# Kernel optimization log

Measured on AMD Instinct MI355X. Metric: run time of the kernel, lower is better.

## Reference

```python
import jax, jax.numpy as jnp
import numpy as np

MODES = 16
WIDTH = 20


def _spectral_conv(x, w_re, w_im):
    # x: (B, C, S) real. Truncated-mode spectral conv: rfft -> keep MODES ->
    # complex channel mixing -> irfft with zero-padded spectrum (numpy irfft
    # zero-pads the input spectrum to n//2+1, matching the torch zero-init out_ft).
    S = x.shape[-1]
    x_ft = jnp.fft.rfft(x, axis=-1)                      # (B, C, S//2+1) complex
    W = w_re + 1j * w_im                                  # (Cin, Cout, MODES)
    out_modes = jnp.einsum('bim,iom->bom', x_ft[:, :, :MODES], W)
    return jnp.fft.irfft(out_modes, n=S, axis=-1)         # (B, Cout, S) real


def _fno(x, point_data,
         fc0_w, fc0_b,
         sw0_re, sw0_im, w0_w, w0_b,
         sw1_re, sw1_im, w1_w, w1_b,
         sw2_re, sw2_im, w2_w, w2_b,
         sw3_re, sw3_im, w3_w, w3_b,
         fc1_w, fc1_b, fc2_w, fc2_b):
    B, S, _ = x.shape
    grid = (point_data / jnp.max(point_data)).reshape(1, S, 1)
    grid = jnp.broadcast_to(grid, (B, S, 1))
    h = jnp.concatenate([x, grid], axis=-1)               # (B, S, 2)
    h = h @ fc0_w + fc0_b                                 # (B, S, W)
    h = jnp.transpose(h, (0, 2, 1))                       # (B, W, S)
    for (sre, sim, ww, wb) in ((sw0_re, sw0_im, w0_w, w0_b),
                               (sw1_re, sw1_im, w1_w, w1_b),
                               (sw2_re, sw2_im, w2_w, w2_b),
                               (sw3_re, sw3_im, w3_w, w3_b)):
        h1 = _spectral_conv(h, sre, sim)
        h2 = jnp.einsum('bcx,oc->box', h, ww) + wb[None, :, None]  # 1x1 conv
        h = jax.nn.gelu(h1 + h2, approximate=False)
    # last layer has no gelu in torch code? It does: only first 3 followed by gelu.
    # Correction handled below.
    return h


def _fno_full(x, point_data,
              fc0_w, fc0_b,
              sw0_re, sw0_im, w0_w, w0_b,
              sw1_re, sw1_im, w1_w, w1_b,
              sw2_re, sw2_im, w2_w, w2_b,
              sw3_re, sw3_im, w3_w, w3_b,
              fc1_w, fc1_b, fc2_w, fc2_b):
    B, S, _ = x.shape
    grid = (point_data / jnp.max(point_data)).reshape(1, S, 1)
    grid = jnp.broadcast_to(grid, (B, S, 1))
    h = jnp.concatenate([x, grid], axis=-1)               # (B, S, 2)
    h = h @ fc0_w + fc0_b                                 # (B, S, W)
    h = jnp.transpose(h, (0, 2, 1))                       # (B, W, S)
    layers = ((sw0_re, sw0_im, w0_w, w0_b),
              (sw1_re, sw1_im, w1_w, w1_b),
              (sw2_re, sw2_im, w2_w, w2_b),
              (sw3_re, sw3_im, w3_w, w3_b))
    for i, (sre, sim, ww, wb) in enumerate(layers):
        h1 = _spectral_conv(h, sre, sim)
        h2 = jnp.einsum('bcx,oc->box', h, ww) + wb[None, :, None]
        h = h1 + h2
        if i < 3:  # torch: gelu after layers 0,1,2 but NOT after layer 3
            h = jax.nn.gelu(h, approximate=False)
    h = jnp.transpose(h, (0, 2, 1))                       # (B, S, W)
    h = jax.nn.gelu(h @ fc1_w + fc1_b, approximate=False)  # (B, S, 128)
    return h @ fc2_w + fc2_b                               # (B, S, 1)


def setup_inputs() -> dict:
    key = jax.random.key(0)
    ks = jax.random.split(key, 32)
    B, S, W, M, H = 32, 65536, WIDTH, MODES, 128
    scale = 1.0 / (W * W)
    d = {
        'x': jax.random.normal(ks[0], (B, S, 1), dtype=jnp.float32),
        'point_data': jax.random.uniform(ks[1], (S,), dtype=jnp.float32),
        'fc0_w': jax.random.normal(ks[2], (2, W), dtype=jnp.float32) * 0.5,
        'fc0_b': jnp.zeros((W,), dtype=jnp.float32),
        'fc1_w': jax.random.normal(ks[3], (W, H), dtype=jnp.float32) * (1.0 / np.sqrt(W)),
        'fc1_b': jnp.zeros((H,), dtype=jnp.float32),
        'fc2_w': jax.random.normal(ks[4], (H, 1), dtype=jnp.float32) * (1.0 / np.sqrt(H)),
        'fc2_b': jnp.zeros((1,), dtype=jnp.float32),
    }
    for i in range(4):
        d[f'sw{i}_re'] = scale * jax.random.uniform(ks[5 + 4 * i], (W, W, M), dtype=jnp.float32)
        d[f'sw{i}_im'] = scale * jax.random.uniform(ks[6 + 4 * i], (W, W, M), dtype=jnp.float32)
        d[f'w{i}_w'] = jax.random.normal(ks[7 + 4 * i], (W, W), dtype=jnp.float32) * (1.0 / np.sqrt(W))
        d[f'w{i}_b'] = jnp.zeros((W,), dtype=jnp.float32)
    return d


def reference(x, point_data,
              fc0_w, fc0_b,
              sw0_re, sw0_im, w0_w, w0_b,
              sw1_re, sw1_im, w1_w, w1_b,
              sw2_re, sw2_im, w2_w, w2_b,
              sw3_re, sw3_im, w3_w, w3_b,
              fc1_w, fc1_b, fc2_w, fc2_b):
    return _fno_full(x, point_data,
                     fc0_w, fc0_b,
                     sw0_re, sw0_im, w0_w, w0_b,
                     sw1_re, sw1_im, w1_w, w1_b,
                     sw2_re, sw2_im, w2_w, w2_b,
                     sw3_re, sw3_im, w3_w, w3_b,
                     fc1_w, fc1_b, fc2_w, fc2_b)
```

## Files before the change

kernel.cpp:

```cpp
#include <hip/hip_runtime.h>
#include <math.h>

#define BB 32
#define SS 65536
#define CC 20
#define NM 16
#define HH 128
#define SP 256
#define WP 64
#define NSLOT 16
#define HREC 12

using short8  = __attribute__((ext_vector_type(8))) short;
using floatx4 = __attribute__((ext_vector_type(4))) float;
using floatx2 = __attribute__((ext_vector_type(2))) float;

__device__ __forceinline__ unsigned short f2bf(float f) {
    union { float f; unsigned u; } v; v.f = f;
    unsigned u = v.u;
    return (unsigned short)((u + 0x7FFFu + ((u >> 16) & 1u)) >> 16);
}
__device__ __forceinline__ float bf2f(unsigned short h) {
    union { unsigned u; float f; } v; v.u = ((unsigned)h) << 16; return v.f;
}
__device__ __forceinline__ unsigned short f2bflo(float a) {
    return f2bf(a - bf2f(f2bf(a)));
}
__device__ __forceinline__ unsigned pk2(unsigned short lo, unsigned short hi) {
    return (unsigned)lo | ((unsigned)hi << 16);
}
__device__ __forceinline__ float asf(unsigned u) {
    union { unsigned u; float f; } v; v.u = u; return v.f;
}
__device__ __forceinline__ unsigned cvtpk(float lo, float hi) {
    unsigned r;
    asm("v_cvt_pk_bf16_f32 %0, %1, %2" : "=v"(r) : "v"(lo), "v"(hi));
    return r;
}

__device__ __forceinline__ float gelu_fast(float v) {
    float u = v * v;
    float inner = v * fmaf(0.0356774081f, u, 0.7978845608f);
    float e = __builtin_amdgcn_exp2f(inner * 2.8853900818f);
    float r = __builtin_amdgcn_rcpf(e + 1.0f);
    return fmaf(-v, r, v);
}

__device__ __forceinline__ floatx2 gelu2(floatx2 v) {
    floatx2 u = v * v;
    floatx2 inner = v * (u * 0.0356774081f + 0.7978845608f);
    floatx2 z = inner * 2.8853900818f;
    floatx2 e, r;
    e.x = __builtin_amdgcn_exp2f(z.x);
    e.y = __builtin_amdgcn_exp2f(z.y);
    r.x = __builtin_amdgcn_rcpf(e.x + 1.0f);
    r.y = __builtin_amdgcn_rcpf(e.y + 1.0f);
    return v - v * r;
}

__device__ __forceinline__ float row16_sum(float p) {
    union { float f; int i; } v, w;
    v.f = p;
    w.i = __builtin_amdgcn_update_dpp(0, v.i, 0x121, 0xF, 0xF, true); v.f += w.f;
    w.i = __builtin_amdgcn_update_dpp(0, v.i, 0x122, 0xF, 0xF, true); v.f += w.f;
    w.i = __builtin_amdgcn_update_dpp(0, v.i, 0x124, 0xF, 0xF, true); v.f += w.f;
    w.i = __builtin_amdgcn_update_dpp(0, v.i, 0x128, 0xF, 0xF, true); v.f += w.f;
    return v.f;
}

__device__ __forceinline__ int swzi(int row, int scol) {
    return row * SP + ((((scol >> 3) ^ row) & 7) << 3) + (scol & 7);
}

__device__ __forceinline__ void stage_A(unsigned short* AST, int tid,
                                        const unsigned* hw,
                                        uint4 tc0, uint4 tc1, uint4 ts0, uint4 ts1) {
    int sw = tid & 7;
    unsigned* base = (unsigned*)(AST + tid * 64);
    *(uint4*)(base + ((0 ^ sw) << 2)) = (uint4){hw[0], hw[1], hw[2], hw[3]};
    *(uint4*)(base + ((1 ^ sw) << 2)) = (uint4){hw[4], hw[5], hw[6], hw[7]};
    *(uint4*)(base + ((2 ^ sw) << 2)) = (uint4){hw[8], hw[9], 0x00003F80u, 0u};
    *(uint4*)(base + ((3 ^ sw) << 2)) = (uint4){0u, 0u, 0u, 0u};
    *(uint4*)(base + ((4 ^ sw) << 2)) = tc0;
    *(uint4*)(base + ((5 ^ sw) << 2)) = tc1;
    *(uint4*)(base + ((6 ^ sw) << 2)) = ts0;
    *(uint4*)(base + ((7 ^ sw) << 2)) = ts1;
}

__global__ __launch_bounds__(256) void k_prep(const float* __restrict__ pd,
                                              const float* __restrict__ w1,
                                              const float* __restrict__ b1f,
                                              float* __restrict__ invmax,
                                              float* __restrict__ cP,
                                              unsigned short* __restrict__ w1Tg,
                                              unsigned* __restrict__ trigT) {
    int bx = blockIdx.x;
    if (bx == 0) {
        __shared__ float red[256];
        int t = threadIdx.x;
        float m = -1e30f;
        for (int i = t; i < SS; i += 256) m = fmaxf(m, pd[i]);
        red[t] = m; __syncthreads();
        for (int off = 128; off > 0; off >>= 1) {
            if (t < off) red[t] = fmaxf(red[t], red[t + off]);
            __syncthreads();
        }
        if (t == 0) invmax[0] = 1.0f / red[0];
    } else if (bx <= 1280) {
        int idx = (bx - 1) * 256 + threadIdx.x;
        float4 z = {0.f, 0.f, 0.f, 0.f};
        ((float4*)cP)[idx] = z;
    } else if (bx == 1281) {
        for (int idx = threadIdx.x; idx < HH * 64; idx += 256) {
            int j = idx >> 6, k = idx & 63;
            unsigned short r = 0;
            if (k < CC) r = f2bf(w1[k * HH + j]);
            else if (k == CC) r = f2bf(b1f[j]);
            else if (k >= 32 && k < 32 + CC) r = f2bflo(w1[(k - 32) * HH + j]);
            else if (k == 32 + CC) r = f2bflo(b1f[j]);
            w1Tg[idx] = r;
        }
    } else {
        int s = (bx - 1282) * 256 + threadIdx.x;
        float u = (float)s * (1.0f / 32768.0f);
        float s1, c1; sincospif(u, &s1, &c1);
        float cm = 1.0f, sm = 0.0f;
        unsigned short ch[NM], sh[NM];
        #pragma unroll
        for (int m = 0; m < NM; ++m) {
            ch[m] = f2bf(cm); sh[m] = f2bf(sm);
            float cn = cm * c1 - sm * s1;
            sm = sm * c1 + cm * s1;
            cm = cn;
        }
        uint4* row = (uint4*)(trigT + (size_t)s * 16);
        row[0] = (uint4){pk2(ch[0],ch[1]), pk2(ch[2],ch[3]), pk2(ch[4],ch[5]), pk2(ch[6],ch[7])};
        row[1] = (uint4){pk2(ch[8],ch[9]), pk2(ch[10],ch[11]), pk2(ch[12],ch[13]), pk2(ch[14],ch[15])};
        row[2] = (uint4){pk2(sh[0],sh[1]), pk2(sh[2],sh[3]), pk2(sh[4],sh[5]), pk2(sh[6],sh[7])};
        row[3] = (uint4){pk2(sh[8],sh[9]), pk2(sh[10],sh[11]), pk2(sh[12],sh[13]), pk2(sh[14],sh[15])};
    }
}

__device__ __forceinline__ void dft_phase(unsigned short* sh_hA, unsigned short* sh_ph,
                                          int tid, float* cPdst) {
    int wave = tid >> 6, lane = tid & 63;
    int quad = lane >> 4, frow = lane & 15;
    floatx4 acc00 = {0.f,0.f,0.f,0.f}, acc01 = {0.f,0.f,0.f,0.f};
    floatx4 acc10 = {0.f,0.f,0.f,0.f}, acc11 = {0.f,0.f,0.f,0.f};
    int kb = wave * 64 + quad * 8;
    #pragma unroll
    for (int kc = 0; kc < 2; ++kc) {
        int k = kb + kc * 32;
        int co = (((k >> 3) ^ frow) & 7) << 3;
        short8 a0 = *(const short8*)(sh_hA + frow * SP + co);
        short8 a1 = *(const short8*)(sh_hA + (16 + frow) * SP + co);
        short8 bc = *(const short8*)(sh_ph + frow * SP + co);
        short8 bs = *(const short8*)(sh_ph + (16 + frow) * SP + co);
        acc00 = __builtin_amdgcn_mfma_f32_16x16x32_bf16(a0, bc, acc00, 0, 0, 0);
        acc01 = __builtin_amdgcn_mfma_f32_16x16x32_bf16(a0, bs, acc01, 0, 0, 0);
        acc10 = __builtin_amdgcn_mfma_f32_16x16x32_bf16(a1, bc, acc10, 0, 0, 0);
        acc11 = __builtin_amdgcn_mfma_f32_16x16x32_bf16(a1, bs, acc11, 0, 0, 0);
    }
    __syncthreads();
    float* red = (float*)sh_hA;
    #pragma unroll
    for (int r = 0; r < 4; ++r) {
        red[wave * 1024 + 0 * 256 + r * 64 + lane] = acc00[r];
        red[wave * 1024 + 1 * 256 + r * 64 + lane] = acc01[r];
        red[wave * 1024 + 2 * 256 + r * 64 + lane] = acc10[r];
        red[wave * 1024 + 3 * 256 + r * 64 + lane] = acc11[r];
    }
    __syncthreads();
    #pragma unroll
    for (int ii = 0; ii < 4; ++ii) {
        int idx = ii * 256 + tid;
        float v = red[idx] + red[1024 + idx] + red[2048 + idx] + red[3072 + idx];
        int f = idx >> 8;
        int r = (idx >> 6) & 3, ln = idx & 63;
        int o = (f >> 1) * 16 + (ln >> 4) * 4 + r;
        int m = ln & 15;
        if (o < CC) atomicAdd(cPdst + (f & 1) * 320 + o * 16 + m, v);
    }
}

__global__ __launch_bounds__(256, 4) void k_fc0_dft(const float* __restrict__ x,
        const float* __restrict__ pd, const float* __restrict__ w,
        const float* __restrict__ bias, const float* __restrict__ invmax,
        const unsigned* __restrict__ trigT,
        unsigned* __restrict__ h2, float* __restrict__ cP0) {
    __shared__ __align__(16) unsigned short LB[2 * 32 * SP];
    unsigned short* sh_hA = LB;
    unsigned short* sh_ph = LB + 32 * SP;
    int tid = threadIdx.x;
    int b = blockIdx.y;
    int s = blockIdx.x * 256 + tid;
    float xv = x[(size_t)b * SS + s];
    float g  = pd[s] * invmax[0];
    const uint4* trow = (const uint4*)(trigT + (size_t)s * 16);
    uint4 tc0 = trow[0], tc1 = trow[1], ts0 = trow[2], ts1 = trow[3];
    unsigned c8[8] = {tc0.x, tc0.y, tc0.z, tc0.w, tc1.x, tc1.y, tc1.z, tc1.w};
    unsigned s8[8] = {ts0.x, ts0.y, ts0.z, ts0.w, ts1.x, ts1.y, ts1.z, ts1.w};
    #pragma unroll
    for (int m = 0; m < NM; ++m) {
        unsigned cd = c8[m >> 1], sd = s8[m >> 1];
        sh_ph[swzi(m, tid)]      = (unsigned short)((m & 1) ? (cd >> 16) : (cd & 0xFFFFu));
        sh_ph[swzi(16 + m, tid)] = (unsigned short)((m & 1) ? (sd >> 16) : (sd & 0xFFFFu));
    }
    unsigned hv[CC / 2];
    #pragma unroll
    for (int p = 0; p < CC / 2; ++p) {
        int c0 = 2 * p, c1i = 2 * p + 1;
        floatx2 wv = {w[c0], w[c1i]};
        floatx2 gv = {w[CC + c0], w[CC + c1i]};
        floatx2 bv = {bias[c0], bias[c1i]};
        floatx2 v = wv * xv + gv * g + bv;
        unsigned dw = cvtpk(v.x, v.y);
        hv[p] = dw;
        sh_hA[swzi(c0, tid)]  = (unsigned short)(dw & 0xFFFFu);
        sh_hA[swzi(c1i, tid)] = (unsigned short)(dw >> 16);
    }
    unsigned* hp2 = h2 + ((size_t)b * SS + s) * HREC;
    *(uint4*)(hp2)     = (uint4){hv[0], hv[1], hv[2], hv[3]};
    *(uint4*)(hp2 + 4) = (uint4){hv[4], hv[5], hv[6], hv[7]};
    *(uint2*)(hp2 + 8) = make_uint2(hv[8], hv[9]);
    __syncthreads();
    dft_phase(sh_hA, sh_ph, tid, cP0 + ((size_t)(blockIdx.x & (NSLOT - 1)) * BB + b) * 640);
}

__global__ __launch_bounds__(256, 4) void k_point_dft(unsigned* __restrict__ h2,
        const unsigned short* __restrict__ Bpk,
        const unsigned* __restrict__ trigT,
        float* __restrict__ cPn) {
    __shared__ __align__(16) unsigned short LB[2 * 32 * SP];
    unsigned short* AST   = LB;
    unsigned short* sh_hA = LB;
    unsigned short* sh_ph = LB + 32 * SP;
    int tid = threadIdx.x;
    int b = blockIdx.y;
    int s = blockIdx.x * 256 + tid;

    const uint4* trow = (const uint4*)(trigT + (size_t)s * 16);
    uint4 tc0 = trow[0], tc1 = trow[1], ts0 = trow[2], ts1 = trow[3];
    const unsigned* hp2r = h2 + ((size_t)b * SS + s) * HREC;
    uint4 h03 = *(const uint4*)(hp2r);
    uint4 h47 = *(const uint4*)(hp2r + 4);
    uint2 h89 = *(const uint2*)(hp2r + 8);
    unsigned hw[CC / 2] = {h03.x, h03.y, h03.z, h03.w, h47.x, h47.y, h47.z, h47.w, h89.x, h89.y};
    stage_A(AST, tid, hw, tc0, tc1, ts0, ts1);

    int wave = tid >> 6, lane = tid & 63, col = lane & 15, quad = lane >> 4;
    const unsigned short* Bp = Bpk + (size_t)b * 4096;
    short8 wh0[2], wh1[2], wl0[2], wl1[2];
    #pragma unroll
    for (int cht = 0; cht < 2; ++cht) {
        int o = cht * 16 + col;
        wh0[cht] = *(const short8*)(Bp + o * 64 + quad * 8);
        wh1[cht] = *(const short8*)(Bp + o * 64 + 32 + quad * 8);
        wl0[cht] = *(const short8*)(Bp + 2048 + o * 64 + quad * 8);
        wl1[cht] = *(const short8*)(Bp + 2048 + o * 64 + 32 + quad * 8);
    }
    unsigned* h2b = h2 + ((size_t)b * SS + blockIdx.x * 256) * HREC;
    unsigned pkr[2][4][2];
    #pragma unroll
    for (int st = 0; st < 4; ++st) {
        int ar = wave * 64 + st * 16 + col;
        int sw = ar & 7;
        const unsigned short* abase = AST + ar * 64;
        short8 ah0 = *(const short8*)(abase + ((quad ^ sw) << 3));
        short8 ah1 = *(const short8*)(abase + (((4 + quad) ^ sw) << 3));
        #pragma unroll
        for (int cht = 0; cht < 2; ++cht) {
            floatx4 a = {0.f, 0.f, 0.f, 0.f};
            a = __builtin_amdgcn_mfma_f32_16x16x32_bf16(wh0[cht], ah0, a, 0, 0, 0);
            a = __builtin_amdgcn_mfma_f32_16x16x32_bf16(wh1[cht], ah1, a, 0, 0, 0);
            a = __builtin_amdgcn_mfma_f32_16x16x32_bf16(wl0[cht], ah0, a, 0, 0, 0);
            a = __builtin_amdgcn_mfma_f32_16x16x32_bf16(wl1[cht], ah1, a, 0, 0, 0);
            floatx2 g01 = gelu2((floatx2){a[0], a[1]});
            floatx2 g23 = gelu2((floatx2){a[2], a[3]});
            unsigned d0 = cvtpk(g01.x, g01.y);
            unsigned d1 = cvtpk(g23.x, g23.y);
            pkr[cht][st][0] = d0;
            pkr[cht][st][1] = d1;
            int p = cht * 8 + quad * 2;
            if (p < CC / 2) {
                *(uint2*)(h2b + (size_t)ar * HREC + p) = make_uint2(d0, d1);
            }
        }
    }
    __syncthreads();

    {
        unsigned c8[8] = {tc0.x, tc0.y, tc0.z, tc0.w, tc1.x, tc1.y, tc1.z, tc1.w};
        unsigned s8[8] = {ts0.x, ts0.y, ts0.z, ts0.w, ts1.x, ts1.y, ts1.z, ts1.w};
        #pragma unroll
        for (int m = 0; m < NM; ++m) {
            unsigned cd = c8[m >> 1], sd = s8[m >> 1];
            sh_ph[swzi(m, tid)]      = (unsigned short)((m & 1) ? (cd >> 16) : (cd & 0xFFFFu));
            sh_ph[swzi(16 + m, tid)] = (unsigned short)((m & 1) ? (sd >> 16) : (sd & 0xFFFFu));
        }
    }
    #pragma unroll
    for (int cht = 0; cht < 2; ++cht) {
        int ob = cht * 16 + quad * 4;
        if (ob < CC) {
            #pragma unroll
            for (int st = 0; st < 4; ++st) {
                int s_loc = wave * 64 + st * 16 + col;
                #pragma unroll
                for (int rp = 0; rp < 2; ++rp) {
                    unsigned d = pkr[cht][st][rp];
                    sh_hA[swzi(ob + 2 * rp, s_loc)]     = (unsigned short)(d & 0xFFFFu);
                    sh_hA[swzi(ob + 2 * rp + 1, s_loc)] = (unsigned short)(d >> 16);
                }
            }
        }
    }
    __syncthreads();
    dft_phase(sh_hA, sh_ph, tid, cPn + ((size_t)(blockIdx.x & (NSLOT - 1)) * BB + b) * 640);
}

__global__ __launch_bounds__(320) void k_mix(const float* __restrict__ cP,
                                             const float* __restrict__ wre, const float* __restrict__ wim,
                                             const float* __restrict__ ww, const float* __restrict__ wb,
                                             float* __restrict__ cA, float* __restrict__ cB,
                                             unsigned short* __restrict__ Bpk) {
    int b = blockIdx.x, tid = threadIdx.x;
    __shared__ float PQ[640];
    const float* base = cP + (size_t)b * 640;
    int i = tid >> 4, m = tid & 15;
    float sP = 0.f, sQ = 0.f;
    #pragma unroll 4
    for (int sl = 0; sl < NSLOT; ++sl) {
        sP += base[(size_t)sl * BB * 640 + tid];
        sQ += base[(size_t)sl * BB * 640 + 320 + tid];
    }
    PQ[i * 32 + m]      = sP;
    PQ[i * 32 + 16 + m] = sQ;
    __syncthreads();
    int o = i;
    float reY = 0.f, imY = 0.f;
    #pragma unroll
    for (int c = 0; c < CC; ++c) {
        float P = PQ[c * 32 + m], Q = PQ[c * 32 + 16 + m];
        float wr = wre[(size_t)(c * CC + o) * NM + m];
        float wi = wim[(size_t)(c * CC + o) * NM + m];
        reY += P * wr + Q * wi;
        imY += P * wi - Q * wr;
    }
    const float invS = 1.0f / (float)SS;
    float a, bb;
    if (m == 0) { a = reY * invS; bb = 0.0f; }
    else        { a = 2.0f * reY * invS; bb = -2.0f * imY * invS; }
    cA[(size_t)(b * CC + o) * NM + m] = a;
    cB[(size_t)(b * CC + o) * NM + m] = bb;

    unsigned short* Bp = Bpk + (size_t)b * 4096;
    for (int idx = tid; idx < 640; idx += 320) {
        int o8 = idx >> 5, k = idx & 31;
        float v = 0.f;
        if (k < CC) v = ww[o8 * CC + k];
        else if (k == CC) v = wb[o8];
        Bp[o8 * 64 + k]        = f2bf(v);
        Bp[2048 + o8 * 64 + k] = f2bflo(v);
    }
    for (int idx = tid; idx < 768; idx += 320) {
        int o8 = 20 + (idx >> 6), k = idx & 63;
        Bp[o8 * 64 + k] = 0;
        Bp[2048 + o8 * 64 + k] = 0;
    }
    Bp[o * 64 + 32 + m]        = f2bf(a);
    Bp[o * 64 + 48 + m]        = f2bf(bb);
    Bp[2048 + o * 64 + 32 + m] = f2bflo(a);
    Bp[2048 + o * 64 + 48 + m] = f2bflo(bb);
}

__global__ __launch_bounds__(128, 4) void k_point_final(const unsigned* __restrict__ h2,
        const unsigned short* __restrict__ Bpk,
        const unsigned short* __restrict__ w1Tg,
        const float* __restrict__ w2, const float* __restrict__ b2,
        const unsigned* __restrict__ trigT,
        float* __restrict__ out) {
    __shared__ __align__(16) unsigned short AST[128 * 64];
    unsigned short* hT = AST;
    int tid = threadIdx.x;
    int b = blockIdx.y;
    int s = blockIdx.x * 128 + tid;

    const uint4* trow = (const uint4*)(trigT + (size_t)s * 16);
    uint4 tc0 = trow[0], tc1 = trow[1], ts0 = trow[2], ts1 = trow[3];
    const unsigned* hp2r = h2 + ((size_t)b * SS + s) * HREC;
    uint4 h03 = *(const uint4*)(hp2r);
    uint4 h47 = *(const uint4*)(hp2r + 4);
    uint2 h89 = *(const uint2*)(hp2r + 8);
    unsigned hw[CC / 2] = {h03.x, h03.y, h03.z, h03.w, h47.x, h47.y, h47.z, h47.w, h89.x, h89.y};
    stage_A(AST, tid, hw, tc0, tc1, ts0, ts1);

    int wave = tid >> 6, lane = tid & 63, col = lane & 15, quad = lane >> 4;
    const unsigned short* Bp = Bpk + (size_t)b * 4096;
    short8 wh0[2], wh1[2], wl0[2], wl1[2];
    #pragma unroll
    for (int cht = 0; cht < 2; ++cht) {
        int o = cht * 16 + col;
        wh0[cht] = *(const short8*)(Bp + o * 64 + quad * 8);
        wh1[cht] = *(const short8*)(Bp + o * 64 + 32 + quad * 8);
        wl0[cht] = *(const short8*)(Bp + 2048 + o * 64 + quad * 8);
        wl1[cht] = *(const short8*)(Bp + 2048 + o * 64 + 32 + quad * 8);
    }
    float res[2][4][4];
    #pragma unroll
    for (int st = 0; st < 4; ++st) {
        int ar = wave * 64 + st * 16 + col;
        int sw = ar & 7;
        const unsigned short* abase = AST + ar * 64;
        short8 ah0 = *(const short8*)(abase + ((quad ^ sw) << 3));
        short8 ah1 = *(const short8*)(abase + (((4 + quad) ^ sw) << 3));
        #pragma unroll
        for (int cht = 0; cht < 2; ++cht) {
            floatx4 a = {0.f, 0.f, 0.f, 0.f};
            a = __builtin_amdgcn_mfma_f32_16x16x32_bf16(wh0[cht], ah0, a, 0, 0, 0);
            a = __builtin_amdgcn_mfma_f32_16x16x32_bf16(wh1[cht], ah1, a, 0, 0, 0);
            a = __builtin_amdgcn_mfma_f32_16x16x32_bf16(wl0[cht], ah0, a, 0, 0, 0);
            a = __builtin_amdgcn_mfma_f32_16x16x32_bf16(wl1[cht], ah1, a, 0, 0, 0);
            #pragma unroll
            for (int r = 0; r < 4; ++r) res[cht][st][r] = a[r];
        }
    }

    #pragma unroll
    for (int cht = 0; cht < 2; ++cht) {
        #pragma unroll
        for (int st = 0; st < 4; ++st) {
            int row = wave * 64 + st * 16 + col;
            int sw = row & 7;
            unsigned* rb = (unsigned*)(hT + row * WP);
            #pragma unroll
            for (int rp = 0; rp < 2; ++rp) {
                int dwi = cht * 8 + quad * 2 + rp;
                if (dwi <= CC / 2) {
                    float f0, f1;
                    if (dwi == CC / 2) { f0 = 1.0f; f1 = 0.0f; }
                    else { f0 = res[cht][st][2 * rp]; f1 = res[cht][st][2 * rp + 1]; }
                    unsigned hd = cvtpk(f0, f1);
                    float r0 = asf(hd << 16), r1 = asf(hd & 0xFFFF0000u);
                    unsigned ld = cvtpk(f0 - r0, f1 - r1);
                    int chunk = dwi >> 2, pos = dwi & 3;
                    rb[((chunk ^ sw) << 2) + pos]       = hd;
                    rb[(((chunk + 4) ^ sw) << 2) + pos] = ld;
                }
            }
        }
    }

    short8 bhi[8], blo[8];
    #pragma unroll
    for (int nt = 0; nt < 8; ++nt) {
        bhi[nt] = *(const short8*)(w1Tg + (size_t)(nt * 16 + col) * 64 + quad * 8);
        blo[nt] = *(const short8*)(w1Tg + (size_t)(nt * 16 + col) * 64 + 32 + quad * 8);
    }
    float w2r[8];
    #pragma unroll
    for (int nt = 0; nt < 8; ++nt) w2r[nt] = w2[nt * 16 + col];
    float b2v = b2[0];
    #pragma unroll
    for (int mt = 0; mt < 4; ++mt) {
        int srow = wave * 64 + mt * 16 + col;
        int sw = srow & 7;
        short8 ahi = *(const short8*)(hT + srow * WP + ((quad ^ sw) << 3));
        short8 alo = *(const short8*)(hT + srow * WP + (((quad ^ sw) ^ 4) << 3));
        float part[4] = {0.f, 0.f, 0.f, 0.f};
        #pragma unroll
        for (int nt = 0; nt < 8; ++nt) {
            floatx4 a = {0.f, 0.f, 0.f, 0.f};
            a = __builtin_amdgcn_mfma_f32_16x16x32_bf16(ahi, bhi[nt], a, 0, 0, 0);
            a = __builtin_amdgcn_mfma_f32_16x16x32_bf16(ahi, blo[nt], a, 0, 0, 0);
            a = __builtin_amdgcn_mfma_f32_16x16x32_bf16(alo, bhi[nt], a, 0, 0, 0);
            #pragma unroll
            for (int r = 0; r < 4; ++r) {
                float t = gelu_fast(a[r]);
                part[r] += t * w2r[nt];
            }
        }
        #pragma unroll
        for (int r = 0; r < 4; ++r) {
            float p = row16_sum(part[r]);
            if (col == 0) {
                int row = wave * 64 + mt * 16 + quad * 4 + r;
                *(float*)(&hT[row * WP + ((row & 7) << 3)]) = p + b2v;
            }
        }
    }
    __syncthreads();
    out[(size_t)b * SS + blockIdx.x * 128 + tid] = *(const float*)(&hT[tid * WP + ((tid & 7) << 3)]);
}

extern "C" void kernel_launch(void* const* d_in, const int* in_sizes, int n_in,
                              void* d_out, int out_size, void* d_ws, size_t ws_size,
                              hipStream_t stream) {
    (void)in_sizes; (void)n_in; (void)out_size; (void)ws_size;
    const float* x    = (const float*)d_in[0];
    const float* pd   = (const float*)d_in[1];
    const float* fc0w = (const float*)d_in[2];
    const float* fc0b = (const float*)d_in[3];
    const float* fc1w = (const float*)d_in[4];
    const float* fc1b = (const float*)d_in[5];
    const float* fc2w = (const float*)d_in[6];
    const float* fc2b = (const float*)d_in[7];

    char* ws = (char*)d_ws;
    unsigned* h2 = (unsigned*)ws;
    size_t off = (size_t)BB * SS * HREC * 4;
    float* cP = (float*)(ws + off); off += (size_t)4 * NSLOT * BB * 640 * 4;
    float* cA = (float*)(ws + off); off += (size_t)BB * CC * NM * 4;
    float* cB = (float*)(ws + off); off += (size_t)BB * CC * NM * 4;
    float* invmax = (float*)(ws + off); off += 256;
    unsigned short* w1Tg = (unsigned short*)(ws + off); off += (size_t)HH * 64 * 2;
    unsigned short* Bpk  = (unsigned short*)(ws + off); off += (size_t)BB * 4096 * 2;
    unsigned* trigT = (unsigned*)(ws + off); off += (size_t)SS * 16 * 4;
    const size_t CPL = (size_t)NSLOT * BB * 640;

    dim3 gBS(SS / 256, BB);
    dim3 gBF(SS / 128, BB);

    k_prep<<<1538, 256, 0, stream>>>(pd, fc1w, fc1b, invmax, cP, w1Tg, trigT);
    k_fc0_dft<<<gBS, 256, 0, stream>>>(x, pd, fc0w, fc0b, invmax, trigT, h2, cP);

    for (int l = 0; l < 3; ++l) {
        const float* wre = (const float*)d_in[8 + 4 * l];
        const float* wim = (const float*)d_in[9 + 4 * l];
        const float* ww  = (const float*)d_in[10 + 4 * l];
        const float* wb  = (const float*)d_in[11 + 4 * l];
        k_mix<<<BB, 320, 0, stream>>>(cP + (size_t)l * CPL, wre, wim, ww, wb, cA, cB, Bpk);
        k_point_dft<<<gBS, 256, 0, stream>>>(h2, Bpk, trigT, cP + (size_t)(l + 1) * CPL);
    }
    {
        const float* wre = (const float*)d_in[20];
        const float* wim = (const float*)d_in[21];
        const float* ww  = (const float*)d_in[22];
        const float* wb  = (const float*)d_in[23];
        k_mix<<<BB, 320, 0, stream>>>(cP + (size_t)3 * CPL, wre, wim, ww, wb, cA, cB, Bpk);
        k_point_final<<<gBF, 128, 0, stream>>>(h2, Bpk, w1Tg, fc2w, fc2b, trigT, (float*)d_out);
    }
}
```

Measured before the change: 505.8 us.

## Process four 256-point chunks per block, accumulating DFT partials in registers

The fc0 and point-DFT kernels now loop over four consecutive 256-point chunks inside each block. MFMA accumulators carry across chunks, so the shared-memory reduction and global atomicAdds run once per block instead of once per chunk. The grid shrinks by four, which cuts launch tail and atomic contention on the partial slots. In exchange there are fewer blocks for latency hiding and serialized syncthreads between chunks within a block.

```diff
diff --git a/kernel.cpp b/kernel.cpp
--- a/kernel.cpp
+++ b/kernel.cpp
@@ -10,6 +10,7 @@
 #define WP 64
 #define NSLOT 16
 #define HREC 12
+#define CH 4
 
 using short8  = __attribute__((ext_vector_type(8))) short;
 using floatx4 = __attribute__((ext_vector_type(4))) float;
@@ -141,12 +142,12 @@
     }
 }
 
-__device__ __forceinline__ void dft_phase(unsigned short* sh_hA, unsigned short* sh_ph,
-                                          int tid, float* cPdst) {
+__device__ __forceinline__ void dft_mfma(const unsigned short* sh_hA,
+                                         const unsigned short* sh_ph, int tid,
+                                         floatx4& acc00, floatx4& acc01,
+                                         floatx4& acc10, floatx4& acc11) {
     int wave = tid >> 6, lane = tid & 63;
     int quad = lane >> 4, frow = lane & 15;
-    floatx4 acc00 = {0.f,0.f,0.f,0.f}, acc01 = {0.f,0.f,0.f,0.f};
-    floatx4 acc10 = {0.f,0.f,0.f,0.f}, acc11 = {0.f,0.f,0.f,0.f};
     int kb = wave * 64 + quad * 8;
     #pragma unroll
     for (int kc = 0; kc < 2; ++kc) {
@@ -161,8 +162,15 @@
         acc10 = __builtin_amdgcn_mfma_f32_16x16x32_bf16(a1, bc, acc10, 0, 0, 0);
         acc11 = __builtin_amdgcn_mfma_f32_16x16x32_bf16(a1, bs, acc11, 0, 0, 0);
     }
+}
+
+__device__ __forceinline__ void dft_reduce(unsigned short* LB, int tid,
+                                           floatx4 acc00, floatx4 acc01,
+                                           floatx4 acc10, floatx4 acc11,
+                                           float* cPdst) {
+    int wave = tid >> 6, lane = tid & 63;
     __syncthreads();
-    float* red = (float*)sh_hA;
+    float* red = (float*)LB;
     #pragma unroll
     for (int r = 0; r < 4; ++r) {
         red[wave * 1024 + 0 * 256 + r * 64 + lane] = acc00[r];
@@ -193,38 +201,47 @@
     unsigned short* sh_ph = LB + 32 * SP;
     int tid = threadIdx.x;
     int b = blockIdx.y;
-    int s = blockIdx.x * 256 + tid;
-    float xv = x[(size_t)b * SS + s];
-    float g  = pd[s] * invmax[0];
-    const uint4* trow = (const uint4*)(trigT + (size_t)s * 16);
-    uint4 tc0 = trow[0], tc1 = trow[1], ts0 = trow[2], ts1 = trow[3];
-    unsigned c8[8] = {tc0.x, tc0.y, tc0.z, tc0.w, tc1.x, tc1.y, tc1.z, tc1.w};
-    unsigned s8[8] = {ts0.x, ts0.y, ts0.z, ts0.w, ts1.x, ts1.y, ts1.z, ts1.w};
-    #pragma unroll
-    for (int m = 0; m < NM; ++m) {
-        unsigned cd = c8[m >> 1], sd = s8[m >> 1];
-        sh_ph[swzi(m, tid)]      = (unsigned short)((m & 1) ? (cd >> 16) : (cd & 0xFFFFu));
-        sh_ph[swzi(16 + m, tid)] = (unsigned short)((m & 1) ? (sd >> 16) : (sd & 0xFFFFu));
-    }
-    unsigned hv[CC / 2];
-    #pragma unroll
-    for (int p = 0; p < CC / 2; ++p) {
-        int c0 = 2 * p, c1i = 2 * p + 1;
-        floatx2 wv = {w[c0], w[c1i]};
-        floatx2 gv = {w[CC + c0], w[CC + c1i]};
-        floatx2 bv = {bias[c0], bias[c1i]};
-        floatx2 v = wv * xv + gv * g + bv;
-        unsigned dw = cvtpk(v.x, v.y);
-        hv[p] = dw;
-        sh_hA[swzi(c0, tid)]  = (unsigned short)(dw & 0xFFFFu);
-        sh_hA[swzi(c1i, tid)] = (unsigned short)(dw >> 16);
-    }
-    unsigned* hp2 = h2 + ((size_t)b * SS + s) * HREC;
-    *(uint4*)(hp2)     = (uint4){hv[0], hv[1], hv[2], hv[3]};
-    *(uint4*)(hp2 + 4) = (uint4){hv[4], hv[5], hv[6], hv[7]};
-    *(uint2*)(hp2 + 8) = make_uint2(hv[8], hv[9]);
-    __syncthreads();
-    dft_phase(sh_hA, sh_ph, tid, cP0 + ((size_t)(blockIdx.x & (NSLOT - 1)) * BB + b) * 640);
+    float im = invmax[0];
+    floatx4 acc00 = {0.f,0.f,0.f,0.f}, acc01 = {0.f,0.f,0.f,0.f};
+    floatx4 acc10 = {0.f,0.f,0.f,0.f}, acc11 = {0.f,0.f,0.f,0.f};
+    #pragma unroll 1
+    for (int chk = 0; chk < CH; ++chk) {
+        if (chk) __syncthreads();
+        int s = blockIdx.x * (256 * CH) + chk * 256 + tid;
+        float xv = x[(size_t)b * SS + s];
+        float g  = pd[s] * im;
+        const uint4* trow = (const uint4*)(trigT + (size_t)s * 16);
+        uint4 tc0 = trow[0], tc1 = trow[1], ts0 = trow[2], ts1 = trow[3];
+        unsigned c8[8] = {tc0.x, tc0.y, tc0.z, tc0.w, tc1.x, tc1.y, tc1.z, tc1.w};
+        unsigned s8[8] = {ts0.x, ts0.y, ts0.z, ts0.w, ts1.x, ts1.y, ts1.z, ts1.w};
+        #pragma unroll
+        for (int m = 0; m < NM; ++m) {
+            unsigned cd = c8[m >> 1], sd = s8[m >> 1];
+            sh_ph[swzi(m, tid)]      = (unsigned short)((m & 1) ? (cd >> 16) : (cd & 0xFFFFu));
+            sh_ph[swzi(16 + m, tid)] = (unsigned short)((m & 1) ? (sd >> 16) : (sd & 0xFFFFu));
+        }
+        unsigned hv[CC / 2];
+        #pragma unroll
+        for (int p = 0; p < CC / 2; ++p) {
+            int c0 = 2 * p, c1i = 2 * p + 1;
+            floatx2 wv = {w[c0], w[c1i]};
+            floatx2 gv = {w[CC + c0], w[CC + c1i]};
+            floatx2 bv = {bias[c0], bias[c1i]};
+            floatx2 v = wv * xv + gv * g + bv;
+            unsigned dw = cvtpk(v.x, v.y);
+            hv[p] = dw;
+            sh_hA[swzi(c0, tid)]  = (unsigned short)(dw & 0xFFFFu);
+            sh_hA[swzi(c1i, tid)] = (unsigned short)(dw >> 16);
+        }
+        unsigned* hp2 = h2 + ((size_t)b * SS + s) * HREC;
+        *(uint4*)(hp2)     = (uint4){hv[0], hv[1], hv[2], hv[3]};
+        *(uint4*)(hp2 + 4) = (uint4){hv[4], hv[5], hv[6], hv[7]};
+        *(uint2*)(hp2 + 8) = make_uint2(hv[8], hv[9]);
+        __syncthreads();
+        dft_mfma(sh_hA, sh_ph, tid, acc00, acc01, acc10, acc11);
+    }
+    dft_reduce(LB, tid, acc00, acc01, acc10, acc11,
+               cP0 + ((size_t)(blockIdx.x & (NSLOT - 1)) * BB + b) * 640);
 }
 
 __global__ __launch_bounds__(256, 4) void k_point_dft(unsigned* __restrict__ h2,
@@ -237,18 +254,8 @@
     unsigned short* sh_ph = LB + 32 * SP;
     int tid = threadIdx.x;
     int b = blockIdx.y;
-    int s = blockIdx.x * 256 + tid;
-
-    const uint4* trow = (const uint4*)(trigT + (size_t)s * 16);
-    uint4 tc0 = trow[0], tc1 = trow[1], ts0 = trow[2], ts1 = trow[3];
-    const unsigned* hp2r = h2 + ((size_t)b * SS + s) * HREC;
-    uint4 h03 = *(const uint4*)(hp2r);
-    uint4 h47 = *(const uint4*)(hp2r + 4);
-    uint2 h89 = *(const uint2*)(hp2r + 8);
-    unsigned hw[CC / 2] = {h03.x, h03.y, h03.z, h03.w, h47.x, h47.y, h47.z, h47.w, h89.x, h89.y};
-    stage_A(AST, tid, hw, tc0, tc1, ts0, ts1);
-
     int wave = tid >> 6, lane = tid & 63, col = lane & 15, quad = lane >> 4;
+
     const unsigned short* Bp = Bpk + (size_t)b * 4096;
     short8 wh0[2], wh1[2], wl0[2], wl1[2];
     #pragma unroll
@@ -259,64 +266,85 @@
         wl0[cht] = *(const short8*)(Bp + 2048 + o * 64 + quad * 8);
         wl1[cht] = *(const short8*)(Bp + 2048 + o * 64 + 32 + quad * 8);
     }
-    unsigned* h2b = h2 + ((size_t)b * SS + blockIdx.x * 256) * HREC;
-    unsigned pkr[2][4][2];
-    #pragma unroll
-    for (int st = 0; st < 4; ++st) {
-        int ar = wave * 64 + st * 16 + col;
-        int sw = ar & 7;
-        const unsigned short* abase = AST + ar * 64;
-        short8 ah0 = *(const short8*)(abase + ((quad ^ sw) << 3));
-        short8 ah1 = *(const short8*)(abase + (((4 + quad) ^ sw) << 3));
-        #pragma unroll
-        for (int cht = 0; cht < 2; ++cht) {
-            floatx4 a = {0.f, 0.f, 0.f, 0.f};
-            a = __builtin_amdgcn_mfma_f32_16x16x32_bf16(wh0[cht], ah0, a, 0, 0, 0);
-            a = __builtin_amdgcn_mfma_f32_16x16x32_bf16(wh1[cht], ah1, a, 0, 0, 0);
-            a = __builtin_amdgcn_mfma_f32_16x16x32_bf16(wl0[cht], ah0, a, 0, 0, 0);
-            a = __builtin_amdgcn_mfma_f32_16x16x32_bf16(wl1[cht], ah1, a, 0, 0, 0);
-            floatx2 g01 = gelu2((floatx2){a[0], a[1]});
-            floatx2 g23 = gelu2((floatx2){a[2], a[3]});
-            unsigned d0 = cvtpk(g01.x, g01.y);
-            unsigned d1 = cvtpk(g23.x, g23.y);
-            pkr[cht][st][0] = d0;
-            pkr[cht][st][1] = d1;
-            int p = cht * 8 + quad * 2;
-            if (p < CC / 2) {
-                *(uint2*)(h2b + (size_t)ar * HREC + p) = make_uint2(d0, d1);
-            }
-        }
-    }
-    __syncthreads();
-
-    {
-        unsigned c8[8] = {tc0.x, tc0.y, tc0.z, tc0.w, tc1.x, tc1.y, tc1.z, tc1.w};
-        unsigned s8[8] = {ts0.x, ts0.y, ts0.z, ts0.w, ts1.x, ts1.y, ts1.z, ts1.w};
-        #pragma unroll
-        for (int m = 0; m < NM; ++m) {
-            unsigned cd = c8[m >> 1], sd = s8[m >> 1];
-            sh_ph[swzi(m, tid)]      = (unsigned short)((m & 1) ? (cd >> 16) : (cd & 0xFFFFu));
-            sh_ph[swzi(16 + m, tid)] = (unsigned short)((m & 1) ? (sd >> 16) : (sd & 0xFFFFu));
-        }
-    }
-    #pragma unroll
-    for (int cht = 0; cht < 2; ++cht) {
-        int ob = cht * 16 + quad * 4;
-        if (ob < CC) {
+    floatx4 acc00 = {0.f,0.f,0.f,0.f}, acc01 = {0.f,0.f,0.f,0.f};
+    floatx4 acc10 = {0.f,0.f,0.f,0.f}, acc11 = {0.f,0.f,0.f,0.f};
+
+    #pragma unroll 1
+    for (int chk = 0; chk < CH; ++chk) {
+        if (chk) __syncthreads();
+        int sbase = blockIdx.x * (256 * CH) + chk * 256;
+        int s = sbase + tid;
+
+        const uint4* trow = (const uint4*)(trigT + (size_t)s * 16);
+        uint4 tc0 = trow[0], tc1 = trow[1], ts0 = trow[2], ts1 = trow[3];
+        const unsigned* hp2r = h2 + ((size_t)b * SS + s) * HREC;
+        uint4 h03 = *(const uint4*)(hp2r);
+        uint4 h47 = *(const uint4*)(hp2r + 4);
+        uint2 h89 = *(const uint2*)(hp2r + 8);
+        unsigned hw[CC / 2] = {h03.x, h03.y, h03.z, h03.w, h47.x, h47.y, h47.z, h47.w, h89.x, h89.y};
+        stage_A(AST, tid, hw, tc0, tc1, ts0, ts1);
+
+        unsigned* h2b = h2 + ((size_t)b * SS + sbase) * HREC;
+        unsigned pkr[2][4][2];
+        #pragma unroll
+        for (int st = 0; st < 4; ++st) {
+            int ar = wave * 64 + st * 16 + col;
+            int sw = ar & 7;
+            const unsigned short* abase = AST + ar * 64;
+            short8 ah0 = *(const short8*)(abase + ((quad ^ sw) << 3));
+            short8 ah1 = *(const short8*)(abase + (((4 + quad) ^ sw) << 3));
             #pragma unroll
-            for (int st = 0; st < 4; ++st) {
-                int s_loc = wave * 64 + st * 16 + col;
-                #pragma unroll
-                for (int rp = 0; rp < 2; ++rp) {
-                    unsigned d = pkr[cht][st][rp];
-                    sh_hA[swzi(ob + 2 * rp, s_loc)]     = (unsigned short)(d & 0xFFFFu);
-                    sh_hA[swzi(ob + 2 * rp + 1, s_loc)] = (unsigned short)(d >> 16);
+            for (int cht = 0; cht < 2; ++cht) {
+                floatx4 a = {0.f, 0.f, 0.f, 0.f};
+                a = __builtin_amdgcn_mfma_f32_16x16x32_bf16(wh0[cht], ah0, a, 0, 0, 0);
+                a = __builtin_amdgcn_mfma_f32_16x16x32_bf16(wh1[cht], ah1, a, 0, 0, 0);
+                a = __builtin_amdgcn_mfma_f32_16x16x32_bf16(wl0[cht], ah0, a, 0, 0, 0);
+                a = __builtin_amdgcn_mfma_f32_16x16x32_bf16(wl1[cht], ah1, a, 0, 0, 0);
+                floatx2 g01 = gelu2((floatx2){a[0], a[1]});
+                floatx2 g23 = gelu2((floatx2){a[2], a[3]});
+                unsigned d0 = cvtpk(g01.x, g01.y);
+                unsigned d1 = cvtpk(g23.x, g23.y);
+                pkr[cht][st][0] = d0;
+                pkr[cht][st][1] = d1;
+                int p = cht * 8 + quad * 2;
+                if (p < CC / 2) {
+                    *(uint2*)(h2b + (size_t)ar * HREC + p) = make_uint2(d0, d1);
                 }
             }
         }
-    }
-    __syncthreads();
-    dft_phase(sh_hA, sh_ph, tid, cPn + ((size_t)(blockIdx.x & (NSLOT - 1)) * BB + b) * 640);
+        __syncthreads();
+
+        {
+            unsigned c8[8] = {tc0.x, tc0.y, tc0.z, tc0.w, tc1.x, tc1.y, tc1.z, tc1.w};
+            unsigned s8[8] = {ts0.x, ts0.y, ts0.z, ts0.w, ts1.x, ts1.y, ts1.z, ts1.w};
+            #pragma unroll
+            for (int m = 0; m < NM; ++m) {
+                unsigned cd = c8[m >> 1], sd = s8[m >> 1];
+                sh_ph[swzi(m, tid)]      = (unsigned short)((m & 1) ? (cd >> 16) : (cd & 0xFFFFu));
+                sh_ph[swzi(16 + m, tid)] = (unsigned short)((m & 1) ? (sd >> 16) : (sd & 0xFFFFu));
+            }
+        }
+        #pragma unroll
+        for (int cht = 0; cht < 2; ++cht) {
+            int ob = cht * 16 + quad * 4;
+            if (ob < CC) {
+                #pragma unroll
+                for (int st = 0; st < 4; ++st) {
+                    int s_loc = wave * 64 + st * 16 + col;
+                    #pragma unroll
+                    for (int rp = 0; rp < 2; ++rp) {
+                        unsigned d = pkr[cht][st][rp];
+                        sh_hA[swzi(ob + 2 * rp, s_loc)]     = (unsigned short)(d & 0xFFFFu);
+                        sh_hA[swzi(ob + 2 * rp + 1, s_loc)] = (unsigned short)(d >> 16);
+                    }
+                }
+            }
+        }
+        __syncthreads();
+        dft_mfma(sh_hA, sh_ph, tid, acc00, acc01, acc10, acc11);
+    }
+    dft_reduce(LB, tid, acc00, acc01, acc10, acc11,
+               cPn + ((size_t)(blockIdx.x & (NSLOT - 1)) * BB + b) * 640);
 }
 
 __global__ __launch_bounds__(320) void k_mix(const float* __restrict__ cP,
@@ -518,7 +546,7 @@
     unsigned* trigT = (unsigned*)(ws + off); off += (size_t)SS * 16 * 4;
     const size_t CPL = (size_t)NSLOT * BB * 640;
 
-    dim3 gBS(SS / 256, BB);
+    dim3 gBS(SS / (256 * CH), BB);
     dim3 gBF(SS / 128, BB);
 
     k_prep<<<1538, 256, 0, stream>>>(pd, fc1w, fc1b, invmax, cP, w1Tg, trigT);
```

New measurement: 705.1 us. 1.39x slower.
